# Optimization experiments

Hardware: AMD Instinct MI355X
Metric: run time of the kernel (lower is better)

The kernel has to match this reference:

```python
import jax, jax.numpy as jnp
import numpy as np

N, E, DIN, H, EIN, EH, STEPS = 10000, 100000, 64, 64, 16, 128, 3


def setup_inputs() -> dict:
    key = jax.random.key(0)
    ks = jax.random.split(key, 8)
    n_feat = jax.random.normal(ks[0], (N, DIN), jnp.float32)
    e_feat = jax.random.normal(ks[1], (E, EIN), jnp.float32)
    src = jax.random.randint(ks[2], (E,), 0, N, jnp.int32)
    dst = jax.random.randint(ks[3], (E,), 0, N, jnp.int32)
    W0 = jax.random.normal(ks[4], (DIN, H), jnp.float32) / np.sqrt(DIN)
    b0 = jnp.zeros((H,), jnp.float32)
    We1 = jax.random.normal(ks[5], (EIN, EH), jnp.float32) / np.sqrt(EIN)
    be1 = jnp.zeros((EH,), jnp.float32)
    # small scale so per-edge HxH weight matrices keep activations stable
    We2 = jax.random.normal(ks[6], (EH, H * H), jnp.float32) * 0.02
    be2 = jnp.zeros((H * H,), jnp.float32)
    conv_bias = jnp.zeros((H,), jnp.float32)
    gamma = jnp.ones((H,), jnp.float32)
    beta = jnp.zeros((H,), jnp.float32)
    return {"n_feat": n_feat, "e_feat": e_feat, "src": src, "dst": dst,
            "W0": W0, "b0": b0, "We1": We1, "be1": be1, "We2": We2,
            "be2": be2, "conv_bias": conv_bias, "gamma": gamma, "beta": beta}


def reference(n_feat, e_feat, src, dst, W0, b0, We1, be1, We2, be2, conv_bias, gamma, beta):
    n = n_feat.shape[0]
    h = W0.shape[1]
    out = jax.nn.relu(n_feat @ W0 + b0)  # [N,H]
    # edge network (eval mode: dropout = identity); e_feat is fixed so the
    # per-edge weight matrices are identical each step -> compute once.
    w_edge = (jax.nn.relu(e_feat @ We1 + be1) @ We2 + be2).reshape(-1, h, h)  # [E,H,H]
    for _ in range(STEPS):
        msg = jnp.einsum('ei,eio->eo', out[src], w_edge)  # gather + per-edge matmul
        agg = jax.ops.segment_sum(msg, dst, num_segments=n)  # scatter-sum to dst
        out = jax.nn.relu(agg + conv_bias)
    # BatchNorm1d over nodes (training-mode batch statistics)
    mean = jnp.mean(out, axis=0)
    var = jnp.var(out, axis=0)
    return (out - mean) * jax.lax.rsqrt(var + 1e-5) * gamma + beta
```

## Files before the change

### kernel.cpp

```cpp
#include <hip/hip_runtime.h>
#include <stdint.h>

#define DIN   64
#define HDIM  64
#define EIN   16
#define EHID  128
#define HH    4096
#define TC    8256
#define STEPS 3

typedef short bf16x8 __attribute__((ext_vector_type(8)));
typedef float f32x4  __attribute__((ext_vector_type(4)));

__device__ __forceinline__ unsigned short f32_to_bf16(float f) {
    union { float f; uint32_t u; } v; v.f = f;
    uint32_t r = v.u + 0x7fffu + ((v.u >> 16) & 1u);
    return (unsigned short)(r >> 16);
}
__device__ __forceinline__ float bfu_to_f(unsigned short u) {
    union { uint32_t u; float f; } v; v.u = (uint32_t)u << 16; return v.f;
}

__global__ void k_pro(const float* __restrict__ nf, const float* __restrict__ W0,
                      const float* __restrict__ b0, float* __restrict__ outb,
                      unsigned short* __restrict__ outbf,
                      const float* __restrict__ ef, const float* __restrict__ We1,
                      const float* __restrict__ be1, unsigned short* __restrict__ h,
                      const float* __restrict__ We2, const float* __restrict__ be2,
                      unsigned short* __restrict__ BmatT,
                      const int* __restrict__ src, const int* __restrict__ dst,
                      int* __restrict__ cntS, int* __restrict__ cntD,
                      int n_nodes, int n_edges, int nbN, int nbE, int nbB) {
    __shared__ float smem[DIN * HDIM];
    int b = blockIdx.x, tid = threadIdx.x;
    if (b < nbN) {
        for (int i = tid; i < DIN * HDIM; i += 256) smem[i] = W0[i];
        __syncthreads();
        int node = b * 4 + (tid >> 6);
        int o = tid & 63;
        if (node >= n_nodes) return;
        float xr = nf[node * DIN + o];
        float acc = b0[o];
#pragma unroll 8
        for (int i = 0; i < DIN; ++i)
            acc += __shfl(xr, i, 64) * smem[i * HDIM + o];
        float v = fmaxf(acc, 0.f);
        outb[node * HDIM + o] = v;
        outbf[node * HDIM + o] = f32_to_bf16(v);
    } else if (b < nbN + nbE) {
        int wave = tid >> 6, lane = tid & 63;
        int r = lane & 15, q = lane >> 4;
        int e0 = (b - nbN) * 64 + wave * 16;
        if (e0 >= n_edges) return;
        bf16x8 afr = (bf16x8){};
        bf16x8 bfr[8];
#pragma unroll
        for (int nt = 0; nt < 8; ++nt) bfr[nt] = (bf16x8){};
        if (q < 2) {
            int ea = e0 + r; if (ea >= n_edges) ea = n_edges - 1;
            const float* xa = ef + (size_t)ea * EIN + q * 8;
#pragma unroll
            for (int j = 0; j < 8; ++j) afr[j] = (short)f32_to_bf16(xa[j]);
#pragma unroll
            for (int nt = 0; nt < 8; ++nt)
#pragma unroll
                for (int j = 0; j < 8; ++j)
                    bfr[nt][j] = (short)f32_to_bf16(We1[(q * 8 + j) * EHID + nt * 16 + r]);
        }
        f32x4 acc[8];
#pragma unroll
        for (int nt = 0; nt < 8; ++nt)
            acc[nt] = __builtin_amdgcn_mfma_f32_16x16x32_bf16(afr, bfr[nt], (f32x4){}, 0, 0, 0);
        float bias[8];
#pragma unroll
        for (int nt = 0; nt < 8; ++nt) bias[nt] = be1[nt * 16 + r];
#pragma unroll
        for (int rg = 0; rg < 4; ++rg) {
            int e = e0 + q * 4 + rg;
            if (e >= n_edges) continue;
            ushort4 pk0, pk1;
            pk0.x = f32_to_bf16(fmaxf(acc[0][rg] + bias[0], 0.f));
            pk0.y = f32_to_bf16(fmaxf(acc[1][rg] + bias[1], 0.f));
            pk0.z = f32_to_bf16(fmaxf(acc[2][rg] + bias[2], 0.f));
            pk0.w = f32_to_bf16(fmaxf(acc[3][rg] + bias[3], 0.f));
            pk1.x = f32_to_bf16(fmaxf(acc[4][rg] + bias[4], 0.f));
            pk1.y = f32_to_bf16(fmaxf(acc[5][rg] + bias[5], 0.f));
            pk1.z = f32_to_bf16(fmaxf(acc[6][rg] + bias[6], 0.f));
            pk1.w = f32_to_bf16(fmaxf(acc[7][rg] + bias[7], 0.f));
            *(ushort4*)(h + (size_t)e * EHID + 4 * r) = pk0;
            *(ushort4*)(h + (size_t)e * EHID + 64 + 4 * r) = pk1;
        }
    } else if (b < nbN + nbE + nbB) {
        int t = (b - nbN - nbE) * 256 + tid;
        if (t >= TC * 64) return;
        int c = t >> 6, i = t & 63;
        int g = c & 63;
        int m = (c & ~63) + 4 * (g & 15) + (g >> 4);
        float v;
        if (m < 8192) {
            int p = ((m >> 11) << 5) | (m & 31);
            int k = (p & 64) + ((p & 3) << 4) + ((p >> 2) & 15);
            int o = (m >> 5) & 63;
            v = We2[k * HH + i * 64 + o];
        } else {
            v = be2[i * 64 + (m - 8192)];
        }
        BmatT[t] = f32_to_bf16(v);
    } else {
        int e = (b - nbN - nbE - nbB) * 256 + tid;
        if (e >= n_edges) return;
        atomicAdd(&cntS[src[e]], 1);
        atomicAdd(&cntD[dst[e]], 1);
    }
}

__global__ void k_T(const unsigned short* __restrict__ outbf, const unsigned short* __restrict__ BmatT,
                    unsigned short* __restrict__ T, int n0, int n1) {
    int wave = threadIdx.x >> 6, lane = threadIdx.x & 63;
    int r = lane & 15, q = lane >> 4;
    int eb = n0 + blockIdx.y * 128;
    int cb = blockIdx.x * 256 + wave * 64;
    bf16x8 bfr[4][2];
#pragma unroll
    for (int nt = 0; nt < 4; ++nt) {
        int c = cb + nt * 16 + r;
        if (c >= TC) c = 0;
        size_t cofs = (size_t)c * 64;
        bfr[nt][0] = *(const bf16x8*)(BmatT + cofs + q * 8);
        bfr[nt][1] = *(const bf16x8*)(BmatT + cofs + 32 + q * 8);
    }
    bool cok = (cb < TC);
#pragma unroll
    for (int mt = 0; mt < 8; ++mt) {
        int e = eb + mt * 16 + r;
        if (e >= n1) e = n1 - 1;
        bf16x8 afr0 = *(const bf16x8*)(outbf + (size_t)e * 64 + q * 8);
        bf16x8 afr1 = *(const bf16x8*)(outbf + (size_t)e * 64 + 32 + q * 8);
        f32x4 acc[4] = {};
#pragma unroll
        for (int nt = 0; nt < 4; ++nt) {
            acc[nt] = __builtin_amdgcn_mfma_f32_16x16x32_bf16(afr0, bfr[nt][0], acc[nt], 0, 0, 0);
            acc[nt] = __builtin_amdgcn_mfma_f32_16x16x32_bf16(afr1, bfr[nt][1], acc[nt], 0, 0, 0);
        }
        if (!cok) continue;
#pragma unroll
        for (int rg = 0; rg < 4; ++rg) {
            int n = eb + mt * 16 + q * 4 + rg;
            if (n >= n1) continue;
            ushort4 pk;
            pk.x = f32_to_bf16(acc[0][rg]);
            pk.y = f32_to_bf16(acc[1][rg]);
            pk.z = f32_to_bf16(acc[2][rg]);
            pk.w = f32_to_bf16(acc[3][rg]);
            *(ushort4*)(T + (size_t)(n - n0) * TC + cb + 4 * r) = pk;
        }
    }
}

__global__ void k_msg(const unsigned short* __restrict__ h, const unsigned short* __restrict__ T,
                      const int* __restrict__ offS, const int* __restrict__ permS,
                      float* __restrict__ msg, int n0, int n1) {
    int wave = threadIdx.x >> 6, lane = threadIdx.x & 63;
    int n = n0 + blockIdx.x * 4 + wave;
    if (n >= n1) return;
    int beg = offS[n], end = offS[n + 1];
    if (beg == end) return;
    int r = lane & 15, q = lane >> 4;
    const unsigned short* Tb = T + (size_t)(n - n0) * TC;
    float bias[4];
#pragma unroll
    for (int nt = 0; nt < 4; ++nt)
        bias[nt] = bfu_to_f(Tb[8192 + nt * 16 + r]);
    for (int j0 = beg; j0 < end; j0 += 16) {
        int jc = j0 + r; if (jc >= end) jc = end - 1;
        int e = permS[jc];
        const unsigned short* he = h + (size_t)e * EHID;
        f32x4 acc[4] = {};
#pragma unroll
        for (int s = 0; s < 4; ++s) {
            bf16x8 afr = *(const bf16x8*)(he + s * 32 + q * 8);
#pragma unroll
            for (int nt = 0; nt < 4; ++nt) {
                bf16x8 bfr = *(const bf16x8*)(Tb + s * 2048 + (nt * 16 + r) * 32 + q * 8);
                acc[nt] = __builtin_amdgcn_mfma_f32_16x16x32_bf16(afr, bfr, acc[nt], 0, 0, 0);
            }
        }
#pragma unroll
        for (int rg = 0; rg < 4; ++rg) {
            int jr = j0 + q * 4 + rg;
            if (jr >= end) continue;
            int er = permS[jr];
#pragma unroll
            for (int nt = 0; nt < 4; ++nt)
                msg[(size_t)er * 64 + nt * 16 + r] = acc[nt][rg] + bias[nt];
        }
    }
}

__global__ void k_scan(const int* __restrict__ cntS, const int* __restrict__ cntD,
                       int* __restrict__ offS, int* __restrict__ offD,
                       int* __restrict__ curS, int* __restrict__ curD, int n, int total) {
    const int* cnt = blockIdx.x ? cntD : cntS;
    int* off = blockIdx.x ? offD : offS;
    int* cur = blockIdx.x ? curD : curS;
    __shared__ int part[256];
    int tid = threadIdx.x;
    int chunk = (n + 255) / 256;
    int c0 = tid * chunk, c1 = c0 + chunk; if (c1 > n) c1 = n; if (c0 > n) c0 = n;
    int s = 0;
    for (int i = c0; i < c1; ++i) s += cnt[i];
    part[tid] = s;
    __syncthreads();
    for (int st = 1; st < 256; st <<= 1) {
        int v = (tid >= st) ? part[tid - st] : 0;
        __syncthreads();
        part[tid] += v;
        __syncthreads();
    }
    int run = tid ? part[tid - 1] : 0;
    for (int i = c0; i < c1; ++i) { off[i] = run; cur[i] = run; run += cnt[i]; }
    if (tid == 0) off[n] = total;
}

__global__ void k_perm(const int* __restrict__ src, const int* __restrict__ dst,
                       int* __restrict__ curS, int* __restrict__ curD,
                       int* __restrict__ permS, int* __restrict__ permD, int n_edges) {
    int e = blockIdx.x * 256 + threadIdx.x;
    if (e >= n_edges) return;
    permS[atomicAdd(&curS[src[e]], 1)] = e;
    permD[atomicAdd(&curD[dst[e]], 1)] = e;
}

__global__ void k_agg(const float* __restrict__ msg, const int* __restrict__ offD,
                      const int* __restrict__ permD, const float* __restrict__ cbias,
                      float* __restrict__ outb, unsigned short* __restrict__ outbf, int n_nodes) {
    int wave = threadIdx.x >> 6, lane = threadIdx.x & 63;
    int d = blockIdx.x * 4 + wave;
    if (d >= n_nodes) return;
    float acc = 0.f;
    int end = offD[d + 1];
    for (int j = offD[d]; j < end; ++j)
        acc += msg[(size_t)permD[j] * 64 + lane];
    float v = fmaxf(acc + cbias[lane], 0.f);
    outb[(size_t)d * 64 + lane] = v;
    outbf[(size_t)d * 64 + lane] = f32_to_bf16(v);
}

__global__ void k_bn_stats(const float* __restrict__ out, float* __restrict__ stat, int n_nodes) {
    __shared__ float s1[256], s2[256];
    int tid = threadIdx.x;
    int f = tid & 63, g = tid >> 6;
    float sum = 0.f, ss = 0.f;
    for (int r = blockIdx.x * 4 + g; r < n_nodes; r += 256) {
        float v = out[r * HDIM + f];
        sum += v; ss += v * v;
    }
    s1[tid] = sum; s2[tid] = ss;
    __syncthreads();
    if (tid < 64) {
        float A = s1[tid] + s1[64 + tid] + s1[128 + tid] + s1[192 + tid];
        float B = s2[tid] + s2[64 + tid] + s2[128 + tid] + s2[192 + tid];
        atomicAdd(&stat[tid], A);
        atomicAdd(&stat[64 + tid], B);
    }
}

__global__ void k_bn_apply(const float* __restrict__ out, const float* __restrict__ stat,
                           const float* __restrict__ gamma, const float* __restrict__ beta,
                           float* __restrict__ y, int n, int n_nodes) {
    int t = blockIdx.x * 256 + threadIdx.x;
    if (t >= n) return;
    int f = t & 63;
    float mean = stat[f] / n_nodes;
    float var  = stat[64 + f] / n_nodes - mean * mean;
    float inv  = rsqrtf(var + 1e-5f);
    float scale = gamma[f] * inv;
    float shift = beta[f] - mean * scale;
    y[t] = out[t] * scale + shift;
}

extern "C" void kernel_launch(void* const* d_in, const int* in_sizes, int n_in,
                              void* d_out, int out_size, void* d_ws, size_t ws_size,
                              hipStream_t stream) {
    const float* nf    = (const float*)d_in[0];
    const float* ef    = (const float*)d_in[1];
    const int*   src   = (const int*)d_in[2];
    const int*   dst   = (const int*)d_in[3];
    const float* W0    = (const float*)d_in[4];
    const float* b0    = (const float*)d_in[5];
    const float* We1   = (const float*)d_in[6];
    const float* be1   = (const float*)d_in[7];
    const float* We2   = (const float*)d_in[8];
    const float* be2   = (const float*)d_in[9];
    const float* cbias = (const float*)d_in[10];
    const float* gamma = (const float*)d_in[11];
    const float* beta  = (const float*)d_in[12];
    (void)n_in; (void)out_size;

    int n_nodes = in_sizes[0] / DIN;
    int n_edges = in_sizes[2];

    char* ws = (char*)d_ws;
    size_t off = 0;
    auto carve = [&](size_t bytes) -> void* {
        void* p = ws + off;
        off = (off + bytes + 255) & ~(size_t)255;
        return p;
    };
    unsigned short* h     = (unsigned short*)carve((size_t)n_edges * EHID * 2);
    float*          msg   = (float*)carve((size_t)n_edges * 64 * 4);
    float*          outb  = (float*)carve((size_t)n_nodes * HDIM * 4);
    unsigned short* outbf = (unsigned short*)carve((size_t)n_nodes * HDIM * 2);
    unsigned short* BmatT = (unsigned short*)carve((size_t)TC * 64 * 2);
    int*            offS  = (int*)carve((size_t)(n_nodes + 1) * 4);
    int*            offD  = (int*)carve((size_t)(n_nodes + 1) * 4);
    int*            curS  = (int*)carve((size_t)n_nodes * 4);
    int*            curD  = (int*)carve((size_t)n_nodes * 4);
    int*            permS = (int*)carve((size_t)n_edges * 4);
    int*            permD = (int*)carve((size_t)n_edges * 4);
    float*          stat  = (float*)carve(128 * 4 + (size_t)2 * n_nodes * 4);
    int*            cntS  = (int*)(stat + 128);
    int*            cntD  = cntS + n_nodes;
    unsigned short* T     = (unsigned short*)(ws + off);
    size_t avail = ws_size > off ? ws_size - off : 0;
    long tcap = (long)(avail / ((size_t)TC * 2));
    if (tcap > n_nodes) tcap = n_nodes;
    if (tcap < 64) tcap = 64;
    long tchunk = tcap;

    hipMemsetAsync(stat, 0, 128 * 4 + (size_t)2 * n_nodes * 4, stream);

    int nbN = (n_nodes + 3) / 4;
    int nbE = (n_edges + 63) / 64;
    int nbB = (TC * 64 + 255) / 256;
    int nbH = (n_edges + 255) / 256;
    k_pro<<<dim3(nbN + nbE + nbB + nbH), 256, 0, stream>>>(
        nf, W0, b0, outb, outbf, ef, We1, be1, h, We2, be2, BmatT,
        src, dst, cntS, cntD, n_nodes, n_edges, nbN, nbE, nbB);
    k_scan<<<dim3(2), 256, 0, stream>>>(cntS, cntD, offS, offD, curS, curD, n_nodes, n_edges);
    k_perm<<<dim3((n_edges + 255) / 256), 256, 0, stream>>>(src, dst, curS, curD, permS, permD, n_edges);

    for (int step = 0; step < STEPS; ++step) {
        for (long n0 = 0; n0 < n_nodes; n0 += tchunk) {
            long n1 = n0 + tchunk; if (n1 > n_nodes) n1 = n_nodes;
            long cnt = n1 - n0;
            k_T<<<dim3((TC + 255) / 256, (cnt + 127) / 128), 256, 0, stream>>>(
                outbf, BmatT, T, (int)n0, (int)n1);
            k_msg<<<dim3((cnt + 3) / 4), 256, 0, stream>>>(
                h, T, offS, permS, msg, (int)n0, (int)n1);
        }
        k_agg<<<dim3((n_nodes + 3) / 4), 256, 0, stream>>>(msg, offD, permD, cbias, outb, outbf, n_nodes);
    }

    k_bn_stats<<<dim3(64), 256, 0, stream>>>(outb, stat, n_nodes);
    k_bn_apply<<<dim3((n_nodes * HDIM + 255) / 256), 256, 0, stream>>>(
        outb, stat, gamma, beta, (float*)d_out, n_nodes * HDIM, n_nodes);
}
```

Baseline: 436.7 us.

## Widen T-kernel column tiles with 16-byte stores and vectorized msg writes

Reorders the BmatT column permutation so each wave in k_T computes 128 columns (8 MFMA tiles) and writes 8 bf16 values per lane as one 16-byte store. The bias tail block is handled separately by a single wave. k_msg now writes four message floats per lane as one float4 in a permuted feature order, and k_agg undoes that permutation when writing node outputs. The intent is fewer, wider global stores and more reuse of the loaded A fragments, at the cost of higher register use for the 8x2 B fragments and eight accumulators.

```diff
diff --git a/kernel.cpp b/kernel.cpp
--- a/kernel.cpp
+++ b/kernel.cpp
@@ -94,8 +94,14 @@
         int t = (b - nbN - nbE) * 256 + tid;
         if (t >= TC * 64) return;
         int c = t >> 6, i = t & 63;
-        int g = c & 63;
-        int m = (c & ~63) + 4 * (g & 15) + (g >> 4);
+        int m;
+        if (c < 8192) {
+            int g = c & 127;
+            m = (c & ~127) + 8 * (g & 15) + (g >> 4);
+        } else {
+            int g = c & 63;
+            m = (c & ~63) + 4 * (g & 15) + (g >> 4);
+        }
         float v;
         if (m < 8192) {
             int p = ((m >> 11) << 5) | (m & 31);
@@ -119,40 +125,74 @@
     int wave = threadIdx.x >> 6, lane = threadIdx.x & 63;
     int r = lane & 15, q = lane >> 4;
     int eb = n0 + blockIdx.y * 128;
-    int cb = blockIdx.x * 256 + wave * 64;
-    bf16x8 bfr[4][2];
-#pragma unroll
-    for (int nt = 0; nt < 4; ++nt) {
-        int c = cb + nt * 16 + r;
-        if (c >= TC) c = 0;
-        size_t cofs = (size_t)c * 64;
-        bfr[nt][0] = *(const bf16x8*)(BmatT + cofs + q * 8);
-        bfr[nt][1] = *(const bf16x8*)(BmatT + cofs + 32 + q * 8);
-    }
-    bool cok = (cb < TC);
-#pragma unroll
-    for (int mt = 0; mt < 8; ++mt) {
-        int e = eb + mt * 16 + r;
-        if (e >= n1) e = n1 - 1;
-        bf16x8 afr0 = *(const bf16x8*)(outbf + (size_t)e * 64 + q * 8);
-        bf16x8 afr1 = *(const bf16x8*)(outbf + (size_t)e * 64 + 32 + q * 8);
-        f32x4 acc[4] = {};
+    if (blockIdx.x < 16) {
+        int cb = blockIdx.x * 512 + wave * 128;
+        bf16x8 bfr[8][2];
+#pragma unroll
+        for (int nt = 0; nt < 8; ++nt) {
+            size_t cofs = (size_t)(cb + nt * 16 + r) * 64;
+            bfr[nt][0] = *(const bf16x8*)(BmatT + cofs + q * 8);
+            bfr[nt][1] = *(const bf16x8*)(BmatT + cofs + 32 + q * 8);
+        }
+#pragma unroll
+        for (int mt = 0; mt < 8; ++mt) {
+            int e = eb + mt * 16 + r;
+            if (e >= n1) e = n1 - 1;
+            bf16x8 afr0 = *(const bf16x8*)(outbf + (size_t)e * 64 + q * 8);
+            bf16x8 afr1 = *(const bf16x8*)(outbf + (size_t)e * 64 + 32 + q * 8);
+            f32x4 acc[8];
+#pragma unroll
+            for (int nt = 0; nt < 8; ++nt) {
+                acc[nt] = __builtin_amdgcn_mfma_f32_16x16x32_bf16(afr0, bfr[nt][0], (f32x4){}, 0, 0, 0);
+                acc[nt] = __builtin_amdgcn_mfma_f32_16x16x32_bf16(afr1, bfr[nt][1], acc[nt], 0, 0, 0);
+            }
+#pragma unroll
+            for (int rg = 0; rg < 4; ++rg) {
+                int n = eb + mt * 16 + q * 4 + rg;
+                if (n >= n1) continue;
+                ushort4 pa, pb;
+                pa.x = f32_to_bf16(acc[0][rg]); pa.y = f32_to_bf16(acc[1][rg]);
+                pa.z = f32_to_bf16(acc[2][rg]); pa.w = f32_to_bf16(acc[3][rg]);
+                pb.x = f32_to_bf16(acc[4][rg]); pb.y = f32_to_bf16(acc[5][rg]);
+                pb.z = f32_to_bf16(acc[6][rg]); pb.w = f32_to_bf16(acc[7][rg]);
+                uint4 pk = { ((uint32_t)pa.y << 16) | pa.x, ((uint32_t)pa.w << 16) | pa.z,
+                             ((uint32_t)pb.y << 16) | pb.x, ((uint32_t)pb.w << 16) | pb.z };
+                *(uint4*)(T + (size_t)(n - n0) * TC + cb + 8 * r) = pk;
+            }
+        }
+    } else {
+        if (wave != 0) return;
+        int cb = 8192;
+        bf16x8 bfr[4][2];
 #pragma unroll
         for (int nt = 0; nt < 4; ++nt) {
-            acc[nt] = __builtin_amdgcn_mfma_f32_16x16x32_bf16(afr0, bfr[nt][0], acc[nt], 0, 0, 0);
-            acc[nt] = __builtin_amdgcn_mfma_f32_16x16x32_bf16(afr1, bfr[nt][1], acc[nt], 0, 0, 0);
-        }
-        if (!cok) continue;
-#pragma unroll
-        for (int rg = 0; rg < 4; ++rg) {
-            int n = eb + mt * 16 + q * 4 + rg;
-            if (n >= n1) continue;
-            ushort4 pk;
-            pk.x = f32_to_bf16(acc[0][rg]);
-            pk.y = f32_to_bf16(acc[1][rg]);
-            pk.z = f32_to_bf16(acc[2][rg]);
-            pk.w = f32_to_bf16(acc[3][rg]);
-            *(ushort4*)(T + (size_t)(n - n0) * TC + cb + 4 * r) = pk;
+            size_t cofs = (size_t)(cb + nt * 16 + r) * 64;
+            bfr[nt][0] = *(const bf16x8*)(BmatT + cofs + q * 8);
+            bfr[nt][1] = *(const bf16x8*)(BmatT + cofs + 32 + q * 8);
+        }
+#pragma unroll
+        for (int mt = 0; mt < 8; ++mt) {
+            int e = eb + mt * 16 + r;
+            if (e >= n1) e = n1 - 1;
+            bf16x8 afr0 = *(const bf16x8*)(outbf + (size_t)e * 64 + q * 8);
+            bf16x8 afr1 = *(const bf16x8*)(outbf + (size_t)e * 64 + 32 + q * 8);
+            f32x4 acc[4];
+#pragma unroll
+            for (int nt = 0; nt < 4; ++nt) {
+                acc[nt] = __builtin_amdgcn_mfma_f32_16x16x32_bf16(afr0, bfr[nt][0], (f32x4){}, 0, 0, 0);
+                acc[nt] = __builtin_amdgcn_mfma_f32_16x16x32_bf16(afr1, bfr[nt][1], acc[nt], 0, 0, 0);
+            }
+#pragma unroll
+            for (int rg = 0; rg < 4; ++rg) {
+                int n = eb + mt * 16 + q * 4 + rg;
+                if (n >= n1) continue;
+                ushort4 pk;
+                pk.x = f32_to_bf16(acc[0][rg]);
+                pk.y = f32_to_bf16(acc[1][rg]);
+                pk.z = f32_to_bf16(acc[2][rg]);
+                pk.w = f32_to_bf16(acc[3][rg]);
+                *(ushort4*)(T + (size_t)(n - n0) * TC + cb + 4 * r) = pk;
+            }
         }
     }
 }
@@ -190,9 +230,9 @@
             int jr = j0 + q * 4 + rg;
             if (jr >= end) continue;
             int er = permS[jr];
-#pragma unroll
-            for (int nt = 0; nt < 4; ++nt)
-                msg[(size_t)er * 64 + nt * 16 + r] = acc[nt][rg] + bias[nt];
+            f32x4 pk = { acc[0][rg] + bias[0], acc[1][rg] + bias[1],
+                         acc[2][rg] + bias[2], acc[3][rg] + bias[3] };
+            *(f32x4*)(msg + (size_t)er * 64 + 4 * r) = pk;
         }
     }
 }
@@ -237,13 +277,14 @@
     int wave = threadIdx.x >> 6, lane = threadIdx.x & 63;
     int d = blockIdx.x * 4 + wave;
     if (d >= n_nodes) return;
+    int o = (lane & 3) * 16 + (lane >> 2);
     float acc = 0.f;
     int end = offD[d + 1];
     for (int j = offD[d]; j < end; ++j)
         acc += msg[(size_t)permD[j] * 64 + lane];
-    float v = fmaxf(acc + cbias[lane], 0.f);
-    outb[(size_t)d * 64 + lane] = v;
-    outbf[(size_t)d * 64 + lane] = f32_to_bf16(v);
+    float v = fmaxf(acc + cbias[o], 0.f);
+    outb[(size_t)d * 64 + o] = v;
+    outbf[(size_t)d * 64 + o] = f32_to_bf16(v);
 }
 
 __global__ void k_bn_stats(const float* __restrict__ out, float* __restrict__ stat, int n_nodes) {
@@ -344,7 +385,7 @@
         for (long n0 = 0; n0 < n_nodes; n0 += tchunk) {
             long n1 = n0 + tchunk; if (n1 > n_nodes) n1 = n_nodes;
             long cnt = n1 - n0;
-            k_T<<<dim3((TC + 255) / 256, (cnt + 127) / 128), 256, 0, stream>>>(
+            k_T<<<dim3(17, (cnt + 127) / 128), 256, 0, stream>>>(
                 outbf, BmatT, T, (int)n0, (int)n1);
             k_msg<<<dim3((cnt + 3) / 4), 256, 0, stream>>>(
                 h, T, offS, permS, msg, (int)n0, (int)n1);
```

Measured after the change: 427.8 us. -2.0%, faster.
